# Kernel optimization log

Hardware: AMD Instinct MI355X
Metric: run time of the kernel (lower is better)

The kernel has to match this reference:

```python
import jax, jax.numpy as jnp
import numpy as np

B, N, F = 32, 1024, 7
HID, HID_GLO, MLP_H, OUT = 256, 8, 64, 8
THRESHOLD = 0.3


def setup_inputs() -> dict:
    key = jax.random.key(0)
    ks = jax.random.split(key, 16)
    def lin(k, fan_out, fan_in):
        # xavier-uniform-like init
        lim = (6.0 / (fan_in + fan_out)) ** 0.5
        return jax.random.uniform(k, (fan_out, fan_in), jnp.float32, -lim, lim)
    return {
        "x": jax.random.normal(ks[0], (B, N, F), jnp.float32),
        "W1": lin(ks[1], HID, 2),   "b1": jnp.zeros((HID,), jnp.float32),
        "W2": lin(ks[2], HID, HID), "b2": jnp.zeros((HID,), jnp.float32),
        "Wfc": lin(ks[3], HID, HID), "bfc": jnp.zeros((HID,), jnp.float32),
        "Wg": lin(ks[4], HID_GLO, 2), "bg": jnp.zeros((HID_GLO,), jnp.float32),
        "Wm0": lin(ks[5], MLP_H, N * F), "bm0": jnp.zeros((MLP_H,), jnp.float32),
        "Wm1": lin(ks[6], MLP_H, MLP_H), "bm1": jnp.zeros((MLP_H,), jnp.float32),
        "Wp": lin(ks[7], OUT, MLP_H + HID + HID_GLO), "bp": jnp.zeros((OUT,), jnp.float32),
    }


def reference(x, W1, b1, W2, b2, Wfc, bfc, Wg, bg, Wm0, bm0, Wm1, bm1, Wp, bp):
    # --- GCN branch (torch code detaches node features & adjacency) ---
    pts = jax.lax.stop_gradient(x[:, :, 1:3])                     # [B,N,2]
    diff = pts[:, :, None, :] - pts[:, None, :, :]                # [B,N,N,2]
    dist = jnp.sqrt(jnp.sum(diff * diff, axis=-1))                # [B,N,N]
    adj = (dist < THRESHOLD).astype(x.dtype)                      # [B,N,N]
    dinv = 1.0 / jnp.sqrt(jnp.sum(adj, axis=-1))                  # [B,N] (>=1, self-loop)
    nadj = dinv[:, :, None] * adj * dinv[:, None, :]              # D^-1/2 A D^-1/2
    h = jax.nn.relu(jnp.einsum('bij,bjd->bid', nadj, pts) @ W1.T + b1)   # [B,N,256]
    g = jnp.einsum('bij,bjh->bih', nadj, h) @ W2.T + b2                  # [B,N,256]
    gcn_en = jnp.mean(g, axis=1) @ Wfc.T + bfc                    # [B,256]

    # --- global branch (torch code uses .item() -> constants) ---
    v = jax.lax.stop_gradient(x[:, :, 1:5])                       # [B,N,4]
    avg_speed = jnp.mean(jnp.linalg.norm(v[:, :, 2:4], axis=-1), axis=1)  # [B]
    density = 1.0 / jnp.max(dist, axis=(1, 2))                    # [B] (v3 == pts)
    glo_in = jnp.stack([avg_speed, density], axis=-1)             # [B,2]
    glo_en = jax.nn.relu(glo_in @ Wg.T + bg)                      # [B,8]

    # --- MLP branch on flattened x ---
    xf = x.reshape(x.shape[0], -1)                                # [B, N*F]
    xf = jax.nn.relu(xf @ Wm0.T + bm0)
    xf = jax.nn.relu(xf @ Wm1.T + bm1)                            # [B,64]

    out = jnp.concatenate([xf, gcn_en, glo_en], axis=1) @ Wp.T + bp  # [B,8]
    return out
```

## Files before the change

kernel.cpp:

```cpp
#include <hip/hip_runtime.h>

#define NN 1024
#define FF 7
#define HID 256
#define MLPH 64
#define OUTN 8
#define CATN (MLPH + HID + 8)

__device__ __forceinline__ float wave_sum(float v) {
#pragma unroll
    for (int m = 32; m >= 1; m >>= 1) v += __shfl_xor(v, m, 64);
    return v;
}
__device__ __forceinline__ float wave_max(float v) {
#pragma unroll
    for (int m = 32; m >= 1; m >>= 1) v = fmaxf(v, __shfl_xor(v, m, 64));
    return v;
}

__global__ __launch_bounds__(512, 2) void g1(const float* __restrict__ x,
                                             const float* __restrict__ Wm0,
                                             const float* __restrict__ W2,
                                             const float* __restrict__ b2,
                                             const float* __restrict__ Wfc,
                                             const float* __restrict__ bfc,
                                             const float* __restrict__ Wp,
                                             float* __restrict__ spd,
                                             float* __restrict__ mlp_p,
                                             float* __restrict__ E,
                                             float* __restrict__ cE,
                                             float* __restrict__ deg,
                                             float* __restrict__ bmaxp,
                                             float* __restrict__ out) {
    __shared__ __align__(16) float lxs[NN * FF];
    __shared__ __align__(16) float l0[NN];
    __shared__ __align__(16) float l1[NN];
    __shared__ __align__(16) float s2[NN];
    __shared__ float wred[8];
    __shared__ float eg0[HID];
    __shared__ float eg1[HID];
    int blk = blockIdx.x, tid = threadIdx.x, lane = tid & 63, w = tid >> 6;
    int b = blk >> 3, jg = blk & 7;

    const float4* wr = (const float4*)(Wm0 + (jg * 8 + w) * (NN * FF));
    float4 wreg[28];
#pragma unroll
    for (int t = 0; t < 28; ++t) wreg[t] = wr[t * 64 + lane];
    const float4* xr4 = (const float4*)(x + b * (NN * FF));
    float4 xreg0 = xr4[tid];
    float4 xreg1 = xr4[512 + tid];
    float4 xreg2 = xr4[1024 + tid];
    float4 xreg3;
    if (tid < 256) xreg3 = xr4[1536 + tid];
    float4* lx4 = (float4*)lxs;
    lx4[tid] = xreg0;
    lx4[512 + tid] = xreg1;
    lx4[1024 + tid] = xreg2;
    if (tid < 256) lx4[1536 + tid] = xreg3;
    __syncthreads();
    l0[tid] = lxs[tid * 7 + 1];       l1[tid] = lxs[tid * 7 + 2];
    l0[tid + 512] = lxs[(tid + 512) * 7 + 1];
    l1[tid + 512] = lxs[(tid + 512) * 7 + 2];
    __syncthreads();
    int jA = jg * 128 + lane, jB = jA + 64;
    float pj0a = l0[jA], pj1a = l1[jA];
    float pj0b = l0[jB], pj1b = l1[jB];
    {
        const float4* v0p = (const float4*)&l0[w * 128];
        const float4* v1p = (const float4*)&l1[w * 128];
        unsigned dA = 0u, dB = 0u;
        float mx = 0.f;
#pragma unroll 4
        for (int g = 0; g < 32; ++g) {
            float4 v0 = v0p[g], v1 = v1p[g];
            float dx, dy, d2a, d2b;
            dx = pj0a - v0.x; dy = pj1a - v1.x; d2a = fmaf(dy, dy, dx * dx);
            dx = pj0b - v0.x; dy = pj1b - v1.x; d2b = fmaf(dy, dy, dx * dx);
            dA += (d2a <= 0.09f); dB += (d2b <= 0.09f);
            mx = fmaxf(mx, fmaxf(d2a, d2b));
            dx = pj0a - v0.y; dy = pj1a - v1.y; d2a = fmaf(dy, dy, dx * dx);
            dx = pj0b - v0.y; dy = pj1b - v1.y; d2b = fmaf(dy, dy, dx * dx);
            dA += (d2a <= 0.09f); dB += (d2b <= 0.09f);
            mx = fmaxf(mx, fmaxf(d2a, d2b));
            dx = pj0a - v0.z; dy = pj1a - v1.z; d2a = fmaf(dy, dy, dx * dx);
            dx = pj0b - v0.z; dy = pj1b - v1.z; d2b = fmaf(dy, dy, dx * dx);
            dA += (d2a <= 0.09f); dB += (d2b <= 0.09f);
            mx = fmaxf(mx, fmaxf(d2a, d2b));
            dx = pj0a - v0.w; dy = pj1a - v1.w; d2a = fmaf(dy, dy, dx * dx);
            dx = pj0b - v0.w; dy = pj1b - v1.w; d2b = fmaf(dy, dy, dx * dx);
            dA += (d2a <= 0.09f); dB += (d2b <= 0.09f);
            mx = fmaxf(mx, fmaxf(d2a, d2b));
        }
        s2[w * 128 + lane] = (float)dA;
        s2[w * 128 + 64 + lane] = (float)dB;
        mx = wave_max(mx);
        if (lane == 0) wred[w] = mx;
    }
    __syncthreads();
    if (tid < 128) {
        float s = 0.f;
#pragma unroll
        for (int kk = 0; kk < 8; ++kk) s += s2[kk * 128 + tid];
        deg[b * NN + jg * 128 + tid] = s;
    }
    if (tid == 0) {
        float m = wred[0];
#pragma unroll
        for (int i = 1; i < 8; ++i) m = fmaxf(m, wred[i]);
        bmaxp[b * 8 + jg] = m;
    }
    {
        float4 a4 = {0.f, 0.f, 0.f, 0.f};
#pragma unroll
        for (int t = 0; t < 28; ++t) {
            float4 xv = lx4[t * 64 + lane];
            a4.x = fmaf(wreg[t].x, xv.x, a4.x);
            a4.y = fmaf(wreg[t].y, xv.y, a4.y);
            a4.z = fmaf(wreg[t].z, xv.z, a4.z);
            a4.w = fmaf(wreg[t].w, xv.w, a4.w);
        }
        float s = (a4.x + a4.y) + (a4.z + a4.w);
        s = wave_sum(s);
        if (lane == 0) mlp_p[b * MLPH + jg * 8 + w] = s;
    }
    __syncthreads();
    if (jg == 0) {
        float vx = lxs[tid * 7 + 3], vy = lxs[tid * 7 + 4];
        float sp = sqrtf(fmaf(vx, vx, vy * vy));
        vx = lxs[(tid + 512) * 7 + 3]; vy = lxs[(tid + 512) * 7 + 4];
        sp += sqrtf(fmaf(vx, vx, vy * vy));
        sp = wave_sum(sp);
        if (lane == 0) wred[w] = sp;
        if (tid < OUTN) out[b * OUTN + tid] = 0.f;
    }
    __syncthreads();
    if (jg == 0 && tid == 0) {
        float s = 0.f;
#pragma unroll
        for (int i = 0; i < 8; ++i) s += wred[i];
        spd[b] = s;
    }
    if (b >= 8 && b < 16 && jg == 7) {
        int o = b - 8;
        int half = tid >> 8, col = tid & 255;
        float* hp = s2;
        if (tid < HID) eg0[tid] = Wp[o * CATN + MLPH + tid];
        __syncthreads();
        {
            float a = 0.f;
            const float* wcol = Wfc + (half * 128) * HID + col;
#pragma unroll 8
            for (int m = 0; m < 128; ++m) a = fmaf(eg0[half * 128 + m], wcol[m * HID], a);
            hp[tid] = a;
        }
        __syncthreads();
        if (tid < HID) eg1[tid] = hp[tid] + hp[tid + 256];
        __syncthreads();
        {
            float e = 0.f;
            const float* wcol = W2 + (half * 128) * HID + col;
#pragma unroll 8
            for (int k = 0; k < 128; ++k) e = fmaf(eg1[half * 128 + k], wcol[k * HID], e);
            hp[tid] = e;
        }
        __syncthreads();
        if (tid < HID) {
            E[o * HID + tid] = hp[tid] + hp[tid + 256];
            float c = fmaf(eg1[tid], b2[tid], eg0[tid] * bfc[tid]);
            c = wave_sum(c);
            if (lane == 0) wred[w] = c;
        }
        __syncthreads();
        if (tid == 0) cE[o] = wred[0] + wred[1] + wred[2] + wred[3];
    }
}

__global__ __launch_bounds__(512, 4) void g2(const float* __restrict__ x,
                                             const float* __restrict__ deg,
                                             const float* __restrict__ W1,
                                             const float* __restrict__ b1,
                                             const float* __restrict__ Wg,
                                             const float* __restrict__ bg,
                                             const float* __restrict__ Wm1,
                                             const float* __restrict__ bm1,
                                             const float* __restrict__ Wp,
                                             const float* __restrict__ bp,
                                             const float* __restrict__ bm0,
                                             const float* __restrict__ mlp_p,
                                             const float* __restrict__ bmaxp,
                                             const float* __restrict__ spd,
                                             const float* __restrict__ E,
                                             const float* __restrict__ cE,
                                             float* __restrict__ out) {
    __shared__ __align__(16) float l0[NN];
    __shared__ __align__(16) float l1[NN];
    __shared__ __align__(16) float di[NN];
    __shared__ __align__(16) float r0[8 * 128];
    __shared__ __align__(16) float r1[8 * 128];
    __shared__ __align__(16) float r2[8 * 128];
    __shared__ __align__(16) float q0s[128];
    __shared__ __align__(16) float q1s[128];
    __shared__ __align__(16) float qws[128];
    __shared__ __align__(16) float hp[512];
    __shared__ float sx1[MLPH], sxf2[MLPH], sglo[8];
    int blk = blockIdx.x, tid = threadIdx.x, lane = tid & 63, w = tid >> 6;
    int b = blk >> 3, jg = blk & 7;
    const float* xb = x + b * (NN * FF);
    {
        int j0 = tid, j1 = tid + 512;
        l0[j0] = xb[j0 * FF + 1]; l1[j0] = xb[j0 * FF + 2];
        l0[j1] = xb[j1 * FF + 1]; l1[j1] = xb[j1 * FF + 2];
        di[j0] = 1.0f / sqrtf(deg[b * NN + j0]);
        di[j1] = 1.0f / sqrtf(deg[b * NN + j1]);
    }
    __syncthreads();
    int jA = jg * 128 + lane, jB = jA + 64;
    float pj0a = l0[jA], pj1a = l1[jA];
    float pj0b = l0[jB], pj1b = l1[jB];
    const float4* v0p = (const float4*)&l0[w * 128];
    const float4* v1p = (const float4*)&l1[w * 128];
    const float4* vdp = (const float4*)&di[w * 128];
    float a0a = 0.f, a1a = 0.f, asa = 0.f;
    float a0b = 0.f, a1b = 0.f, asb = 0.f;
#pragma unroll 4
    for (int g = 0; g < 32; ++g) {
        float4 v0 = v0p[g], v1 = v1p[g], vd = vdp[g];
        float dx, dy, d2, t;
        dx = pj0a - v0.x; dy = pj1a - v1.x; d2 = fmaf(dy, dy, dx * dx);
        t = (d2 <= 0.09f) ? vd.x : 0.0f;
        a0a = fmaf(t, v0.x, a0a); a1a = fmaf(t, v1.x, a1a); asa += t;
        dx = pj0b - v0.x; dy = pj1b - v1.x; d2 = fmaf(dy, dy, dx * dx);
        t = (d2 <= 0.09f) ? vd.x : 0.0f;
        a0b = fmaf(t, v0.x, a0b); a1b = fmaf(t, v1.x, a1b); asb += t;
        dx = pj0a - v0.y; dy = pj1a - v1.y; d2 = fmaf(dy, dy, dx * dx);
        t = (d2 <= 0.09f) ? vd.y : 0.0f;
        a0a = fmaf(t, v0.y, a0a); a1a = fmaf(t, v1.y, a1a); asa += t;
        dx = pj0b - v0.y; dy = pj1b - v1.y; d2 = fmaf(dy, dy, dx * dx);
        t = (d2 <= 0.09f) ? vd.y : 0.0f;
        a0b = fmaf(t, v0.y, a0b); a1b = fmaf(t, v1.y, a1b); asb += t;
        dx = pj0a - v0.z; dy = pj1a - v1.z; d2 = fmaf(dy, dy, dx * dx);
        t = (d2 <= 0.09f) ? vd.z : 0.0f;
        a0a = fmaf(t, v0.z, a0a); a1a = fmaf(t, v1.z, a1a); asa += t;
        dx = pj0b - v0.z; dy = pj1b - v1.z; d2 = fmaf(dy, dy, dx * dx);
        t = (d2 <= 0.09f) ? vd.z : 0.0f;
        a0b = fmaf(t, v0.z, a0b); a1b = fmaf(t, v1.z, a1b); asb += t;
        dx = pj0a - v0.w; dy = pj1a - v1.w; d2 = fmaf(dy, dy, dx * dx);
        t = (d2 <= 0.09f) ? vd.w : 0.0f;
        a0a = fmaf(t, v0.w, a0a); a1a = fmaf(t, v1.w, a1a); asa += t;
        dx = pj0b - v0.w; dy = pj1b - v1.w; d2 = fmaf(dy, dy, dx * dx);
        t = (d2 <= 0.09f) ? vd.w : 0.0f;
        a0b = fmaf(t, v0.w, a0b); a1b = fmaf(t, v1.w, a1b); asb += t;
    }
    r0[w * 128 + lane] = a0a; r0[w * 128 + 64 + lane] = a0b;
    r1[w * 128 + lane] = a1a; r1[w * 128 + 64 + lane] = a1b;
    r2[w * 128 + lane] = asa; r2[w * 128 + 64 + lane] = asb;
    __syncthreads();
    if (tid < 128) {
        float s0 = 0.f, s1 = 0.f, ss = 0.f;
#pragma unroll
        for (int kk = 0; kk < 8; ++kk) {
            s0 += r0[kk * 128 + tid];
            s1 += r1[kk * 128 + tid];
            ss += r2[kk * 128 + tid];
        }
        float dj = di[jg * 128 + tid];
        q0s[tid] = dj * s0;
        q1s[tid] = dj * s1;
        qws[tid] = dj * ss * (1.0f / NN);
    } else if (jg == 0 && tid < 192) {
        int t2 = tid - 128;
        sx1[t2] = fmaxf(mlp_p[b * MLPH + t2] + bm0[t2], 0.f);
    }
    __syncthreads();
    {
        int h = tid & 255, jq = tid >> 8;
        float w10 = W1[2 * h], w11 = W1[2 * h + 1], bb = b1[h];
        const float4* q0v = (const float4*)&q0s[jq * 64];
        const float4* q1v = (const float4*)&q1s[jq * 64];
        const float4* qwv = (const float4*)&qws[jq * 64];
        float acc = 0.f;
#pragma unroll
        for (int g = 0; g < 16; ++g) {
            float4 qa = q0v[g], qb = q1v[g], qw4 = qwv[g];
            acc = fmaf(qw4.x, fmaxf(fmaf(qb.x, w11, fmaf(qa.x, w10, bb)), 0.f), acc);
            acc = fmaf(qw4.y, fmaxf(fmaf(qb.y, w11, fmaf(qa.y, w10, bb)), 0.f), acc);
            acc = fmaf(qw4.z, fmaxf(fmaf(qb.z, w11, fmaf(qa.z, w10, bb)), 0.f), acc);
            acc = fmaf(qw4.w, fmaxf(fmaf(qb.w, w11, fmaf(qa.w, w10, bb)), 0.f), acc);
        }
        hp[jq * 256 + h] = acc;
    }
    __syncthreads();
    if (tid < HID) {
        r0[tid] = hp[tid] + hp[256 + tid];
    } else if (jg == 0 && tid < HID + MLPH) {
        int t2 = tid - HID;
        float a = bm1[t2];
        const float* wv = Wm1 + t2 * MLPH;
#pragma unroll
        for (int k = 0; k < MLPH; ++k) a = fmaf(wv[k], sx1[k], a);
        sxf2[t2] = fmaxf(a, 0.f);
    } else if (jg == 0 && tid < HID + MLPH + 8) {
        int t2 = tid - HID - MLPH;
        float mxv = 0.f;
#pragma unroll
        for (int g = 0; g < 8; ++g) mxv = fmaxf(mxv, bmaxp[b * 8 + g]);
        float avg  = spd[b] * (1.0f / NN);
        float dens = 1.0f / sqrtf(mxv);
        sglo[t2] = fmaxf(fmaf(Wg[t2 * 2], avg, fmaf(Wg[t2 * 2 + 1], dens, bg[t2])), 0.f);
    }
    __syncthreads();
    {
        int o = w, ln = lane;
        const float* Eo = E + o * HID;
        float a = Eo[ln] * r0[ln];
        a = fmaf(Eo[ln + 64],  r0[ln + 64],  a);
        a = fmaf(Eo[ln + 128], r0[ln + 128], a);
        a = fmaf(Eo[ln + 192], r0[ln + 192], a);
        if (jg == 0) a = fmaf(Wp[o * CATN + ln], sxf2[ln], a);
        a = wave_sum(a);
        if (ln == 0) {
            if (jg == 0) {
                const float* wg = Wp + o * CATN + MLPH + HID;
#pragma unroll
                for (int g = 0; g < 8; ++g) a = fmaf(wg[g], sglo[g], a);
                a += cE[o] + bp[o];
            }
            atomicAdd(&out[b * OUTN + o], a);
        }
    }
}

extern "C" void kernel_launch(void* const* d_in, const int* in_sizes, int n_in,
                              void* d_out, int out_size, void* d_ws, size_t ws_size,
                              hipStream_t stream) {
    const float* x   = (const float*)d_in[0];
    const float* W1  = (const float*)d_in[1];
    const float* b1  = (const float*)d_in[2];
    const float* W2  = (const float*)d_in[3];
    const float* b2  = (const float*)d_in[4];
    const float* Wfc = (const float*)d_in[5];
    const float* bfc = (const float*)d_in[6];
    const float* Wg  = (const float*)d_in[7];
    const float* bg  = (const float*)d_in[8];
    const float* Wm0 = (const float*)d_in[9];
    const float* bm0 = (const float*)d_in[10];
    const float* Wm1 = (const float*)d_in[11];
    const float* bm1 = (const float*)d_in[12];
    const float* Wp  = (const float*)d_in[13];
    const float* bp  = (const float*)d_in[14];
    float* out = (float*)d_out;
    float* ws  = (float*)d_ws;

    float* deg   = ws;
    float* mlp_p = ws + 32768;
    float* bmaxp = ws + 34816;
    float* spd   = ws + 35072;
    float* E     = ws + 35104;
    float* cE    = ws + 37152;

    g1<<<256, 512, 0, stream>>>(x, Wm0, W2, b2, Wfc, bfc, Wp,
                                spd, mlp_p, E, cE, deg, bmaxp, out);
    g2<<<256, 512, 0, stream>>>(x, deg, W1, b1, Wg, bg, Wm1, bm1,
                                Wp, bp, bm0, mlp_p, bmaxp, spd, E, cE, out);
}
```

Measured before the change: 113.3 us.

## Fuse two kernels into one with per-batch spin-wait flags and inline W2/Wfc matvecs

Merges the two launches into a single kernel. The 8 blocks of each batch exchange degree, max-distance and MLP partials through global memory, gated by per-block release flags and a bounded spin-wait. The precomputed Wp·Wfc·W2 projection is dropped; each block now runs the W2 and Wfc matvecs on its own partial aggregate. This removes a launch gap and the serial E-precompute path, but relies on all 8 blocks of a batch being co-resident to avoid deadlock, and adds redundant per-block matvec work plus a hand-rolled release/acquire protocol whose ordering is delicate.

```diff
diff --git a/kernel.cpp b/kernel.cpp
--- a/kernel.cpp
+++ b/kernel.cpp
@@ -7,6 +7,9 @@
 #define OUTN 8
 #define CATN (MLPH + HID + 8)
 
+#define FMAGIC 0x9E3779B97F4A7C15ULL
+#define SCOPE_AGENT __HIP_MEMORY_SCOPE_AGENT
+
 __device__ __forceinline__ float wave_sum(float v) {
 #pragma unroll
     for (int m = 32; m >= 1; m >>= 1) v += __shfl_xor(v, m, 64);
@@ -17,30 +20,58 @@
     for (int m = 32; m >= 1; m >>= 1) v = fmaxf(v, __shfl_xor(v, m, 64));
     return v;
 }
-
-__global__ __launch_bounds__(512, 2) void g1(const float* __restrict__ x,
+__device__ __forceinline__ void st_ag(float* p, float v) {
+    __hip_atomic_store(p, v, __ATOMIC_RELAXED, SCOPE_AGENT);
+}
+__device__ __forceinline__ float ld_ag(const float* p) {
+    return __hip_atomic_load(p, __ATOMIC_RELAXED, SCOPE_AGENT);
+}
+
+union SU {
+    float lxs[NN * FF];
+    struct {
+        float r0[NN], r1[NN], r2[NN];
+        float q0s[128], q1s[128], qws[128];
+        float hp[512];
+        float yh[512];
+        float yv[HID];
+        float zv[HID];
+        float sx1[MLPH], sxf2[MLPH], sglo[8];
+    } p2;
+};
+
+__global__ __launch_bounds__(512, 2) void gf(const float* __restrict__ x,
                                              const float* __restrict__ Wm0,
                                              const float* __restrict__ W2,
                                              const float* __restrict__ b2,
                                              const float* __restrict__ Wfc,
                                              const float* __restrict__ bfc,
+                                             const float* __restrict__ W1,
+                                             const float* __restrict__ b1,
+                                             const float* __restrict__ Wg,
+                                             const float* __restrict__ bg,
+                                             const float* __restrict__ Wm1,
+                                             const float* __restrict__ bm1,
                                              const float* __restrict__ Wp,
-                                             float* __restrict__ spd,
+                                             const float* __restrict__ bp,
+                                             const float* __restrict__ bm0,
                                              float* __restrict__ mlp_p,
-                                             float* __restrict__ E,
-                                             float* __restrict__ cE,
                                              float* __restrict__ deg,
                                              float* __restrict__ bmaxp,
+                                             unsigned long long* __restrict__ flags,
                                              float* __restrict__ out) {
-    __shared__ __align__(16) float lxs[NN * FF];
+    __shared__ __align__(16) SU u;
     __shared__ __align__(16) float l0[NN];
     __shared__ __align__(16) float l1[NN];
+    __shared__ __align__(16) float di[NN];
     __shared__ __align__(16) float s2[NN];
     __shared__ float wred[8];
-    __shared__ float eg0[HID];
-    __shared__ float eg1[HID];
+    __shared__ float sspd;
+
     int blk = blockIdx.x, tid = threadIdx.x, lane = tid & 63, w = tid >> 6;
     int b = blk >> 3, jg = blk & 7;
+    unsigned long long* myflag = &flags[b * 8 + jg];
+    if (tid == 0) __hip_atomic_store(myflag, 0ULL, __ATOMIC_RELAXED, SCOPE_AGENT);
 
     const float4* wr = (const float4*)(Wm0 + (jg * 8 + w) * (NN * FF));
     float4 wreg[28];
@@ -52,15 +83,15 @@
     float4 xreg2 = xr4[1024 + tid];
     float4 xreg3;
     if (tid < 256) xreg3 = xr4[1536 + tid];
-    float4* lx4 = (float4*)lxs;
+    float4* lx4 = (float4*)u.lxs;
     lx4[tid] = xreg0;
     lx4[512 + tid] = xreg1;
     lx4[1024 + tid] = xreg2;
     if (tid < 256) lx4[1536 + tid] = xreg3;
     __syncthreads();
-    l0[tid] = lxs[tid * 7 + 1];       l1[tid] = lxs[tid * 7 + 2];
-    l0[tid + 512] = lxs[(tid + 512) * 7 + 1];
-    l1[tid + 512] = lxs[(tid + 512) * 7 + 2];
+    l0[tid] = u.lxs[tid * 7 + 1];       l1[tid] = u.lxs[tid * 7 + 2];
+    l0[tid + 512] = u.lxs[(tid + 512) * 7 + 1];
+    l1[tid + 512] = u.lxs[(tid + 512) * 7 + 2];
     __syncthreads();
     int jA = jg * 128 + lane, jB = jA + 64;
     float pj0a = l0[jA], pj1a = l1[jA];
@@ -101,13 +132,13 @@
         float s = 0.f;
 #pragma unroll
         for (int kk = 0; kk < 8; ++kk) s += s2[kk * 128 + tid];
-        deg[b * NN + jg * 128 + tid] = s;
+        st_ag(&deg[b * NN + jg * 128 + tid], s);
     }
     if (tid == 0) {
         float m = wred[0];
 #pragma unroll
         for (int i = 1; i < 8; ++i) m = fmaxf(m, wred[i]);
-        bmaxp[b * 8 + jg] = m;
+        st_ag(&bmaxp[b * 8 + jg], m);
     }
     {
         float4 a4 = {0.f, 0.f, 0.f, 0.f};
@@ -121,139 +152,84 @@
         }
         float s = (a4.x + a4.y) + (a4.z + a4.w);
         s = wave_sum(s);
-        if (lane == 0) mlp_p[b * MLPH + jg * 8 + w] = s;
+        if (lane == 0) st_ag(&mlp_p[b * MLPH + jg * 8 + w], s);
     }
     __syncthreads();
     if (jg == 0) {
-        float vx = lxs[tid * 7 + 3], vy = lxs[tid * 7 + 4];
+        float vx = u.lxs[tid * 7 + 3], vy = u.lxs[tid * 7 + 4];
         float sp = sqrtf(fmaf(vx, vx, vy * vy));
-        vx = lxs[(tid + 512) * 7 + 3]; vy = lxs[(tid + 512) * 7 + 4];
+        vx = u.lxs[(tid + 512) * 7 + 3]; vy = u.lxs[(tid + 512) * 7 + 4];
         sp += sqrtf(fmaf(vx, vx, vy * vy));
         sp = wave_sum(sp);
         if (lane == 0) wred[w] = sp;
-        if (tid < OUTN) out[b * OUTN + tid] = 0.f;
+        if (tid < OUTN) st_ag(&out[b * OUTN + tid], 0.f);
     }
     __syncthreads();
     if (jg == 0 && tid == 0) {
         float s = 0.f;
 #pragma unroll
         for (int i = 0; i < 8; ++i) s += wred[i];
-        spd[b] = s;
-    }
-    if (b >= 8 && b < 16 && jg == 7) {
-        int o = b - 8;
-        int half = tid >> 8, col = tid & 255;
-        float* hp = s2;
-        if (tid < HID) eg0[tid] = Wp[o * CATN + MLPH + tid];
-        __syncthreads();
-        {
-            float a = 0.f;
-            const float* wcol = Wfc + (half * 128) * HID + col;
-#pragma unroll 8
-            for (int m = 0; m < 128; ++m) a = fmaf(eg0[half * 128 + m], wcol[m * HID], a);
-            hp[tid] = a;
-        }
-        __syncthreads();
-        if (tid < HID) eg1[tid] = hp[tid] + hp[tid + 256];
-        __syncthreads();
-        {
-            float e = 0.f;
-            const float* wcol = W2 + (half * 128) * HID + col;
-#pragma unroll 8
-            for (int k = 0; k < 128; ++k) e = fmaf(eg1[half * 128 + k], wcol[k * HID], e);
-            hp[tid] = e;
-        }
-        __syncthreads();
-        if (tid < HID) {
-            E[o * HID + tid] = hp[tid] + hp[tid + 256];
-            float c = fmaf(eg1[tid], b2[tid], eg0[tid] * bfc[tid]);
-            c = wave_sum(c);
-            if (lane == 0) wred[w] = c;
-        }
-        __syncthreads();
-        if (tid == 0) cE[o] = wred[0] + wred[1] + wred[2] + wred[3];
-    }
-}
-
-__global__ __launch_bounds__(512, 4) void g2(const float* __restrict__ x,
-                                             const float* __restrict__ deg,
-                                             const float* __restrict__ W1,
-                                             const float* __restrict__ b1,
-                                             const float* __restrict__ Wg,
-                                             const float* __restrict__ bg,
-                                             const float* __restrict__ Wm1,
-                                             const float* __restrict__ bm1,
-                                             const float* __restrict__ Wp,
-                                             const float* __restrict__ bp,
-                                             const float* __restrict__ bm0,
-                                             const float* __restrict__ mlp_p,
-                                             const float* __restrict__ bmaxp,
-                                             const float* __restrict__ spd,
-                                             const float* __restrict__ E,
-                                             const float* __restrict__ cE,
-                                             float* __restrict__ out) {
-    __shared__ __align__(16) float l0[NN];
-    __shared__ __align__(16) float l1[NN];
-    __shared__ __align__(16) float di[NN];
-    __shared__ __align__(16) float r0[8 * 128];
-    __shared__ __align__(16) float r1[8 * 128];
-    __shared__ __align__(16) float r2[8 * 128];
-    __shared__ __align__(16) float q0s[128];
-    __shared__ __align__(16) float q1s[128];
-    __shared__ __align__(16) float qws[128];
-    __shared__ __align__(16) float hp[512];
-    __shared__ float sx1[MLPH], sxf2[MLPH], sglo[8];
-    int blk = blockIdx.x, tid = threadIdx.x, lane = tid & 63, w = tid >> 6;
-    int b = blk >> 3, jg = blk & 7;
-    const float* xb = x + b * (NN * FF);
-    {
-        int j0 = tid, j1 = tid + 512;
-        l0[j0] = xb[j0 * FF + 1]; l1[j0] = xb[j0 * FF + 2];
-        l0[j1] = xb[j1 * FF + 1]; l1[j1] = xb[j1 * FF + 2];
-        di[j0] = 1.0f / sqrtf(deg[b * NN + j0]);
-        di[j1] = 1.0f / sqrtf(deg[b * NN + j1]);
-    }
-    __syncthreads();
-    int jA = jg * 128 + lane, jB = jA + 64;
-    float pj0a = l0[jA], pj1a = l1[jA];
-    float pj0b = l0[jB], pj1b = l1[jB];
-    const float4* v0p = (const float4*)&l0[w * 128];
-    const float4* v1p = (const float4*)&l1[w * 128];
-    const float4* vdp = (const float4*)&di[w * 128];
-    float a0a = 0.f, a1a = 0.f, asa = 0.f;
-    float a0b = 0.f, a1b = 0.f, asb = 0.f;
+        sspd = s;
+    }
+    __syncthreads();
+    if (tid == 0)
+        __hip_atomic_store(myflag, FMAGIC, __ATOMIC_RELEASE, SCOPE_AGENT);
+
+    if (tid < 8) {
+        int it = 0;
+        while (__hip_atomic_load(&flags[b * 8 + tid], __ATOMIC_RELAXED,
+                                 SCOPE_AGENT) != FMAGIC && it < (1 << 20)) {
+            __builtin_amdgcn_s_sleep(2);
+            ++it;
+        }
+    }
+    __syncthreads();
+
+    di[tid]       = 1.0f / sqrtf(ld_ag(&deg[b * NN + tid]));
+    di[tid + 512] = 1.0f / sqrtf(ld_ag(&deg[b * NN + tid + 512]));
+    __syncthreads();
+    float* r0 = u.p2.r0;
+    float* r1 = u.p2.r1;
+    float* r2 = u.p2.r2;
+    {
+        const float4* v0p = (const float4*)&l0[w * 128];
+        const float4* v1p = (const float4*)&l1[w * 128];
+        const float4* vdp = (const float4*)&di[w * 128];
+        float a0a = 0.f, a1a = 0.f, asa = 0.f;
+        float a0b = 0.f, a1b = 0.f, asb = 0.f;
 #pragma unroll 4
-    for (int g = 0; g < 32; ++g) {
-        float4 v0 = v0p[g], v1 = v1p[g], vd = vdp[g];
-        float dx, dy, d2, t;
-        dx = pj0a - v0.x; dy = pj1a - v1.x; d2 = fmaf(dy, dy, dx * dx);
-        t = (d2 <= 0.09f) ? vd.x : 0.0f;
-        a0a = fmaf(t, v0.x, a0a); a1a = fmaf(t, v1.x, a1a); asa += t;
-        dx = pj0b - v0.x; dy = pj1b - v1.x; d2 = fmaf(dy, dy, dx * dx);
-        t = (d2 <= 0.09f) ? vd.x : 0.0f;
-        a0b = fmaf(t, v0.x, a0b); a1b = fmaf(t, v1.x, a1b); asb += t;
-        dx = pj0a - v0.y; dy = pj1a - v1.y; d2 = fmaf(dy, dy, dx * dx);
-        t = (d2 <= 0.09f) ? vd.y : 0.0f;
-        a0a = fmaf(t, v0.y, a0a); a1a = fmaf(t, v1.y, a1a); asa += t;
-        dx = pj0b - v0.y; dy = pj1b - v1.y; d2 = fmaf(dy, dy, dx * dx);
-        t = (d2 <= 0.09f) ? vd.y : 0.0f;
-        a0b = fmaf(t, v0.y, a0b); a1b = fmaf(t, v1.y, a1b); asb += t;
-        dx = pj0a - v0.z; dy = pj1a - v1.z; d2 = fmaf(dy, dy, dx * dx);
-        t = (d2 <= 0.09f) ? vd.z : 0.0f;
-        a0a = fmaf(t, v0.z, a0a); a1a = fmaf(t, v1.z, a1a); asa += t;
-        dx = pj0b - v0.z; dy = pj1b - v1.z; d2 = fmaf(dy, dy, dx * dx);
-        t = (d2 <= 0.09f) ? vd.z : 0.0f;
-        a0b = fmaf(t, v0.z, a0b); a1b = fmaf(t, v1.z, a1b); asb += t;
-        dx = pj0a - v0.w; dy = pj1a - v1.w; d2 = fmaf(dy, dy, dx * dx);
-        t = (d2 <= 0.09f) ? vd.w : 0.0f;
-        a0a = fmaf(t, v0.w, a0a); a1a = fmaf(t, v1.w, a1a); asa += t;
-        dx = pj0b - v0.w; dy = pj1b - v1.w; d2 = fmaf(dy, dy, dx * dx);
-        t = (d2 <= 0.09f) ? vd.w : 0.0f;
-        a0b = fmaf(t, v0.w, a0b); a1b = fmaf(t, v1.w, a1b); asb += t;
-    }
-    r0[w * 128 + lane] = a0a; r0[w * 128 + 64 + lane] = a0b;
-    r1[w * 128 + lane] = a1a; r1[w * 128 + 64 + lane] = a1b;
-    r2[w * 128 + lane] = asa; r2[w * 128 + 64 + lane] = asb;
+        for (int g = 0; g < 32; ++g) {
+            float4 v0 = v0p[g], v1 = v1p[g], vd = vdp[g];
+            float dx, dy, d2, t;
+            dx = pj0a - v0.x; dy = pj1a - v1.x; d2 = fmaf(dy, dy, dx * dx);
+            t = (d2 <= 0.09f) ? vd.x : 0.0f;
+            a0a = fmaf(t, v0.x, a0a); a1a = fmaf(t, v1.x, a1a); asa += t;
+            dx = pj0b - v0.x; dy = pj1b - v1.x; d2 = fmaf(dy, dy, dx * dx);
+            t = (d2 <= 0.09f) ? vd.x : 0.0f;
+            a0b = fmaf(t, v0.x, a0b); a1b = fmaf(t, v1.x, a1b); asb += t;
+            dx = pj0a - v0.y; dy = pj1a - v1.y; d2 = fmaf(dy, dy, dx * dx);
+            t = (d2 <= 0.09f) ? vd.y : 0.0f;
+            a0a = fmaf(t, v0.y, a0a); a1a = fmaf(t, v1.y, a1a); asa += t;
+            dx = pj0b - v0.y; dy = pj1b - v1.y; d2 = fmaf(dy, dy, dx * dx);
+            t = (d2 <= 0.09f) ? vd.y : 0.0f;
+            a0b = fmaf(t, v0.y, a0b); a1b = fmaf(t, v1.y, a1b); asb += t;
+            dx = pj0a - v0.z; dy = pj1a - v1.z; d2 = fmaf(dy, dy, dx * dx);
+            t = (d2 <= 0.09f) ? vd.z : 0.0f;
+            a0a = fmaf(t, v0.z, a0a); a1a = fmaf(t, v1.z, a1a); asa += t;
+            dx = pj0b - v0.z; dy = pj1b - v1.z; d2 = fmaf(dy, dy, dx * dx);
+            t = (d2 <= 0.09f) ? vd.z : 0.0f;
+            a0b = fmaf(t, v0.z, a0b); a1b = fmaf(t, v1.z, a1b); asb += t;
+            dx = pj0a - v0.w; dy = pj1a - v1.w; d2 = fmaf(dy, dy, dx * dx);
+            t = (d2 <= 0.09f) ? vd.w : 0.0f;
+            a0a = fmaf(t, v0.w, a0a); a1a = fmaf(t, v1.w, a1a); asa += t;
+            dx = pj0b - v0.w; dy = pj1b - v1.w; d2 = fmaf(dy, dy, dx * dx);
+            t = (d2 <= 0.09f) ? vd.w : 0.0f;
+            a0b = fmaf(t, v0.w, a0b); a1b = fmaf(t, v1.w, a1b); asb += t;
+        }
+        r0[w * 128 + lane] = a0a; r0[w * 128 + 64 + lane] = a0b;
+        r1[w * 128 + lane] = a1a; r1[w * 128 + 64 + lane] = a1b;
+        r2[w * 128 + lane] = asa; r2[w * 128 + 64 + lane] = asb;
+    }
     __syncthreads();
     if (tid < 128) {
         float s0 = 0.f, s1 = 0.f, ss = 0.f;
@@ -264,20 +240,20 @@
             ss += r2[kk * 128 + tid];
         }
         float dj = di[jg * 128 + tid];
-        q0s[tid] = dj * s0;
-        q1s[tid] = dj * s1;
-        qws[tid] = dj * ss * (1.0f / NN);
+        u.p2.q0s[tid] = dj * s0;
+        u.p2.q1s[tid] = dj * s1;
+        u.p2.qws[tid] = dj * ss * (1.0f / NN);
     } else if (jg == 0 && tid < 192) {
         int t2 = tid - 128;
-        sx1[t2] = fmaxf(mlp_p[b * MLPH + t2] + bm0[t2], 0.f);
+        u.p2.sx1[t2] = fmaxf(ld_ag(&mlp_p[b * MLPH + t2]) + bm0[t2], 0.f);
     }
     __syncthreads();
     {
         int h = tid & 255, jq = tid >> 8;
         float w10 = W1[2 * h], w11 = W1[2 * h + 1], bb = b1[h];
-        const float4* q0v = (const float4*)&q0s[jq * 64];
-        const float4* q1v = (const float4*)&q1s[jq * 64];
-        const float4* qwv = (const float4*)&qws[jq * 64];
+        const float4* q0v = (const float4*)&u.p2.q0s[jq * 64];
+        const float4* q1v = (const float4*)&u.p2.q1s[jq * 64];
+        const float4* qwv = (const float4*)&u.p2.qws[jq * 64];
         float acc = 0.f;
 #pragma unroll
         for (int g = 0; g < 16; ++g) {
@@ -287,43 +263,77 @@
             acc = fmaf(qw4.z, fmaxf(fmaf(qb.z, w11, fmaf(qa.z, w10, bb)), 0.f), acc);
             acc = fmaf(qw4.w, fmaxf(fmaf(qb.w, w11, fmaf(qa.w, w10, bb)), 0.f), acc);
         }
-        hp[jq * 256 + h] = acc;
+        u.p2.hp[jq * 256 + h] = acc;
     }
     __syncthreads();
     if (tid < HID) {
-        r0[tid] = hp[tid] + hp[256 + tid];
+        r0[tid] = u.p2.hp[tid] + u.p2.hp[256 + tid];
     } else if (jg == 0 && tid < HID + MLPH) {
         int t2 = tid - HID;
         float a = bm1[t2];
         const float* wv = Wm1 + t2 * MLPH;
 #pragma unroll
-        for (int k = 0; k < MLPH; ++k) a = fmaf(wv[k], sx1[k], a);
-        sxf2[t2] = fmaxf(a, 0.f);
+        for (int k = 0; k < MLPH; ++k) a = fmaf(wv[k], u.p2.sx1[k], a);
+        u.p2.sxf2[t2] = fmaxf(a, 0.f);
     } else if (jg == 0 && tid < HID + MLPH + 8) {
         int t2 = tid - HID - MLPH;
         float mxv = 0.f;
 #pragma unroll
-        for (int g = 0; g < 8; ++g) mxv = fmaxf(mxv, bmaxp[b * 8 + g]);
-        float avg  = spd[b] * (1.0f / NN);
+        for (int g = 0; g < 8; ++g) mxv = fmaxf(mxv, ld_ag(&bmaxp[b * 8 + g]));
+        float avg  = sspd * (1.0f / NN);
         float dens = 1.0f / sqrtf(mxv);
-        sglo[t2] = fmaxf(fmaf(Wg[t2 * 2], avg, fmaf(Wg[t2 * 2 + 1], dens, bg[t2])), 0.f);
-    }
+        u.p2.sglo[t2] = fmaxf(fmaf(Wg[t2 * 2], avg, fmaf(Wg[t2 * 2 + 1], dens, bg[t2])), 0.f);
+    }
+    __syncthreads();
+    {
+        int r = tid >> 1, half = tid & 1;
+        const float4* w4 = (const float4*)(W2 + r * HID + half * 128);
+        const float4* v4 = (const float4*)&r0[half * 128];
+        float acc = 0.f;
+#pragma unroll
+        for (int t = 0; t < 32; ++t) {
+            float4 a = w4[t], vv = v4[t];
+            acc = fmaf(a.x, vv.x, acc); acc = fmaf(a.y, vv.y, acc);
+            acc = fmaf(a.z, vv.z, acc); acc = fmaf(a.w, vv.w, acc);
+        }
+        u.p2.yh[tid] = acc;
+    }
+    __syncthreads();
+    if (tid < HID)
+        u.p2.yv[tid] = u.p2.yh[2 * tid] + u.p2.yh[2 * tid + 1] + (jg == 0 ? b2[tid] : 0.f);
+    __syncthreads();
+    {
+        int r = tid >> 1, half = tid & 1;
+        const float4* w4 = (const float4*)(Wfc + r * HID + half * 128);
+        const float4* v4 = (const float4*)&u.p2.yv[half * 128];
+        float acc = 0.f;
+#pragma unroll
+        for (int t = 0; t < 32; ++t) {
+            float4 a = w4[t], vv = v4[t];
+            acc = fmaf(a.x, vv.x, acc); acc = fmaf(a.y, vv.y, acc);
+            acc = fmaf(a.z, vv.z, acc); acc = fmaf(a.w, vv.w, acc);
+        }
+        u.p2.yh[tid] = acc;
+    }
+    __syncthreads();
+    if (tid < HID)
+        u.p2.zv[tid] = u.p2.yh[2 * tid] + u.p2.yh[2 * tid + 1] + (jg == 0 ? bfc[tid] : 0.f);
     __syncthreads();
     {
         int o = w, ln = lane;
-        const float* Eo = E + o * HID;
-        float a = Eo[ln] * r0[ln];
-        a = fmaf(Eo[ln + 64],  r0[ln + 64],  a);
-        a = fmaf(Eo[ln + 128], r0[ln + 128], a);
-        a = fmaf(Eo[ln + 192], r0[ln + 192], a);
-        if (jg == 0) a = fmaf(Wp[o * CATN + ln], sxf2[ln], a);
+        const float* wpo = Wp + o * CATN;
+        float a = wpo[MLPH + ln] * u.p2.zv[ln];
+        a = fmaf(wpo[MLPH + ln + 64],  u.p2.zv[ln + 64],  a);
+        a = fmaf(wpo[MLPH + ln + 128], u.p2.zv[ln + 128], a);
+        a = fmaf(wpo[MLPH + ln + 192], u.p2.zv[ln + 192], a);
+        if (jg == 0) a = fmaf(wpo[ln], u.p2.sxf2[ln], a);
         a = wave_sum(a);
         if (ln == 0) {
             if (jg == 0) {
-                const float* wg = Wp + o * CATN + MLPH + HID;
-#pragma unroll
-                for (int g = 0; g < 8; ++g) a = fmaf(wg[g], sglo[g], a);
-                a += cE[o] + bp[o];
+                const float* wg = wpo + MLPH + HID;
+#pragma unroll
+                for (int g = 0; g < 8; ++g) a = fmaf(wg[g], u.p2.sglo[g], a);
+                a += bp[o];
             }
             atomicAdd(&out[b * OUTN + o], a);
         }
@@ -354,12 +364,9 @@
     float* deg   = ws;
     float* mlp_p = ws + 32768;
     float* bmaxp = ws + 34816;
-    float* spd   = ws + 35072;
-    float* E     = ws + 35104;
-    float* cE    = ws + 37152;
-
-    g1<<<256, 512, 0, stream>>>(x, Wm0, W2, b2, Wfc, bfc, Wp,
-                                spd, mlp_p, E, cE, deg, bmaxp, out);
-    g2<<<256, 512, 0, stream>>>(x, deg, W1, b1, Wg, bg, Wm1, bm1,
-                                Wp, bp, bm0, mlp_p, bmaxp, spd, E, cE, out);
-}
+    unsigned long long* flags = (unsigned long long*)(ws + 35072);
+
+    gf<<<256, 512, 0, stream>>>(x, Wm0, W2, b2, Wfc, bfc, W1, b1, Wg, bg,
+                                Wm1, bm1, Wp, bp, bm0,
+                                mlp_p, deg, bmaxp, flags, out);
+}
```

Result: slower. 120.0 us (+5.9%).

## Double grid to 16 blocks per batch and stage packed point coordinates

Applied to the files above, without the earlier changes.

Both kernels now use 16 blocks per batch with 64 target nodes each instead of 8 blocks with 128, which halves per-thread work and register use (Wm0 register tile shrinks from 28 to 14 float4). g1 writes de-interleaved x/y coordinates to workspace so g2 can load them with coalesced float4 reads instead of strided gathers from x. The intent is more parallelism and occupancy on a small problem, at the cost of redundantly recomputing all pairwise distances in more blocks and running more partial reductions and atomics.

```diff
diff --git a/kernel.cpp b/kernel.cpp
--- a/kernel.cpp
+++ b/kernel.cpp
@@ -18,7 +18,7 @@
     return v;
 }
 
-__global__ __launch_bounds__(512, 2) void g1(const float* __restrict__ x,
+__global__ __launch_bounds__(512, 4) void g1(const float* __restrict__ x,
                                              const float* __restrict__ Wm0,
                                              const float* __restrict__ W2,
                                              const float* __restrict__ b2,
@@ -31,89 +31,79 @@
                                              float* __restrict__ cE,
                                              float* __restrict__ deg,
                                              float* __restrict__ bmaxp,
+                                             float* __restrict__ pts0,
+                                             float* __restrict__ pts1,
                                              float* __restrict__ out) {
     __shared__ __align__(16) float lxs[NN * FF];
     __shared__ __align__(16) float l0[NN];
     __shared__ __align__(16) float l1[NN];
-    __shared__ __align__(16) float s2[NN];
+    __shared__ __align__(16) float s2[512];
     __shared__ float wred[8];
-    __shared__ float eg0[HID];
-    __shared__ float eg1[HID];
+    __shared__ float mred[8];
+    __shared__ float eg0[HID], eg1[HID];
     int blk = blockIdx.x, tid = threadIdx.x, lane = tid & 63, w = tid >> 6;
-    int b = blk >> 3, jg = blk & 7;
-
-    const float4* wr = (const float4*)(Wm0 + (jg * 8 + w) * (NN * FF));
-    float4 wreg[28];
-#pragma unroll
-    for (int t = 0; t < 28; ++t) wreg[t] = wr[t * 64 + lane];
+    int b = blk >> 4, jq = blk & 15;
+
+    int hrow = jq * 4 + (w >> 1), hsel = w & 1;
+    const float4* wr = (const float4*)(Wm0 + hrow * (NN * FF)) + hsel * 896;
+    float4 wreg[14];
+#pragma unroll
+    for (int t = 0; t < 14; ++t) wreg[t] = wr[t * 64 + lane];
     const float4* xr4 = (const float4*)(x + b * (NN * FF));
-    float4 xreg0 = xr4[tid];
-    float4 xreg1 = xr4[512 + tid];
-    float4 xreg2 = xr4[1024 + tid];
-    float4 xreg3;
-    if (tid < 256) xreg3 = xr4[1536 + tid];
+    float4 x0 = xr4[tid], x1 = xr4[512 + tid], x2 = xr4[1024 + tid], x3;
+    if (tid < 256) x3 = xr4[1536 + tid];
     float4* lx4 = (float4*)lxs;
-    lx4[tid] = xreg0;
-    lx4[512 + tid] = xreg1;
-    lx4[1024 + tid] = xreg2;
-    if (tid < 256) lx4[1536 + tid] = xreg3;
-    __syncthreads();
-    l0[tid] = lxs[tid * 7 + 1];       l1[tid] = lxs[tid * 7 + 2];
+    lx4[tid] = x0;
+    lx4[512 + tid] = x1;
+    lx4[1024 + tid] = x2;
+    if (tid < 256) lx4[1536 + tid] = x3;
+    __syncthreads();
+    l0[tid] = lxs[tid * 7 + 1];        l1[tid] = lxs[tid * 7 + 2];
     l0[tid + 512] = lxs[(tid + 512) * 7 + 1];
     l1[tid + 512] = lxs[(tid + 512) * 7 + 2];
     __syncthreads();
-    int jA = jg * 128 + lane, jB = jA + 64;
-    float pj0a = l0[jA], pj1a = l1[jA];
-    float pj0b = l0[jB], pj1b = l1[jB];
+    int j = jq * 64 + lane;
+    float pj0 = l0[j], pj1 = l1[j];
     {
         const float4* v0p = (const float4*)&l0[w * 128];
         const float4* v1p = (const float4*)&l1[w * 128];
-        unsigned dA = 0u, dB = 0u;
+        unsigned dA = 0u;
         float mx = 0.f;
 #pragma unroll 4
         for (int g = 0; g < 32; ++g) {
             float4 v0 = v0p[g], v1 = v1p[g];
-            float dx, dy, d2a, d2b;
-            dx = pj0a - v0.x; dy = pj1a - v1.x; d2a = fmaf(dy, dy, dx * dx);
-            dx = pj0b - v0.x; dy = pj1b - v1.x; d2b = fmaf(dy, dy, dx * dx);
-            dA += (d2a <= 0.09f); dB += (d2b <= 0.09f);
-            mx = fmaxf(mx, fmaxf(d2a, d2b));
-            dx = pj0a - v0.y; dy = pj1a - v1.y; d2a = fmaf(dy, dy, dx * dx);
-            dx = pj0b - v0.y; dy = pj1b - v1.y; d2b = fmaf(dy, dy, dx * dx);
-            dA += (d2a <= 0.09f); dB += (d2b <= 0.09f);
-            mx = fmaxf(mx, fmaxf(d2a, d2b));
-            dx = pj0a - v0.z; dy = pj1a - v1.z; d2a = fmaf(dy, dy, dx * dx);
-            dx = pj0b - v0.z; dy = pj1b - v1.z; d2b = fmaf(dy, dy, dx * dx);
-            dA += (d2a <= 0.09f); dB += (d2b <= 0.09f);
-            mx = fmaxf(mx, fmaxf(d2a, d2b));
-            dx = pj0a - v0.w; dy = pj1a - v1.w; d2a = fmaf(dy, dy, dx * dx);
-            dx = pj0b - v0.w; dy = pj1b - v1.w; d2b = fmaf(dy, dy, dx * dx);
-            dA += (d2a <= 0.09f); dB += (d2b <= 0.09f);
-            mx = fmaxf(mx, fmaxf(d2a, d2b));
-        }
-        s2[w * 128 + lane] = (float)dA;
-        s2[w * 128 + 64 + lane] = (float)dB;
+            float dx, dy, d2;
+            dx = pj0 - v0.x; dy = pj1 - v1.x; d2 = fmaf(dy, dy, dx * dx);
+            dA += (d2 <= 0.09f); mx = fmaxf(mx, d2);
+            dx = pj0 - v0.y; dy = pj1 - v1.y; d2 = fmaf(dy, dy, dx * dx);
+            dA += (d2 <= 0.09f); mx = fmaxf(mx, d2);
+            dx = pj0 - v0.z; dy = pj1 - v1.z; d2 = fmaf(dy, dy, dx * dx);
+            dA += (d2 <= 0.09f); mx = fmaxf(mx, d2);
+            dx = pj0 - v0.w; dy = pj1 - v1.w; d2 = fmaf(dy, dy, dx * dx);
+            dA += (d2 <= 0.09f); mx = fmaxf(mx, d2);
+        }
+        s2[w * 64 + lane] = (float)dA;
         mx = wave_max(mx);
         if (lane == 0) wred[w] = mx;
     }
     __syncthreads();
-    if (tid < 128) {
+    if (tid < 64) {
         float s = 0.f;
 #pragma unroll
-        for (int kk = 0; kk < 8; ++kk) s += s2[kk * 128 + tid];
-        deg[b * NN + jg * 128 + tid] = s;
+        for (int kk = 0; kk < 8; ++kk) s += s2[kk * 64 + tid];
+        deg[b * NN + jq * 64 + tid] = s;
     }
     if (tid == 0) {
         float m = wred[0];
 #pragma unroll
         for (int i = 1; i < 8; ++i) m = fmaxf(m, wred[i]);
-        bmaxp[b * 8 + jg] = m;
+        bmaxp[b * 16 + jq] = m;
     }
     {
         float4 a4 = {0.f, 0.f, 0.f, 0.f};
 #pragma unroll
-        for (int t = 0; t < 28; ++t) {
-            float4 xv = lx4[t * 64 + lane];
+        for (int t = 0; t < 14; ++t) {
+            float4 xv = lx4[hsel * 896 + t * 64 + lane];
             a4.x = fmaf(wreg[t].x, xv.x, a4.x);
             a4.y = fmaf(wreg[t].y, xv.y, a4.y);
             a4.z = fmaf(wreg[t].z, xv.z, a4.z);
@@ -121,10 +111,12 @@
         }
         float s = (a4.x + a4.y) + (a4.z + a4.w);
         s = wave_sum(s);
-        if (lane == 0) mlp_p[b * MLPH + jg * 8 + w] = s;
-    }
-    __syncthreads();
-    if (jg == 0) {
+        if (lane == 0) mred[w] = s;
+    }
+    __syncthreads();
+    if ((w & 1) == 0 && lane == 0)
+        mlp_p[b * MLPH + hrow] = mred[w] + mred[w + 1];
+    if (jq == 0) {
         float vx = lxs[tid * 7 + 3], vy = lxs[tid * 7 + 4];
         float sp = sqrtf(fmaf(vx, vx, vy * vy));
         vx = lxs[(tid + 512) * 7 + 3]; vy = lxs[(tid + 512) * 7 + 4];
@@ -132,15 +124,19 @@
         sp = wave_sum(sp);
         if (lane == 0) wred[w] = sp;
         if (tid < OUTN) out[b * OUTN + tid] = 0.f;
-    }
-    __syncthreads();
-    if (jg == 0 && tid == 0) {
+        if (tid < 256) {
+            ((float4*)(pts0 + b * NN))[tid] = ((float4*)l0)[tid];
+            ((float4*)(pts1 + b * NN))[tid] = ((float4*)l1)[tid];
+        }
+    }
+    __syncthreads();
+    if (jq == 0 && tid == 0) {
         float s = 0.f;
 #pragma unroll
         for (int i = 0; i < 8; ++i) s += wred[i];
         spd[b] = s;
     }
-    if (b >= 8 && b < 16 && jg == 7) {
+    if (b >= 8 && b < 16 && jq == 15) {
         int o = b - 8;
         int half = tid >> 8, col = tid & 255;
         float* hp = s2;
@@ -175,7 +171,8 @@
     }
 }
 
-__global__ __launch_bounds__(512, 4) void g2(const float* __restrict__ x,
+__global__ __launch_bounds__(512, 4) void g2(const float* __restrict__ pts0,
+                                             const float* __restrict__ pts1,
                                              const float* __restrict__ deg,
                                              const float* __restrict__ W1,
                                              const float* __restrict__ b1,
@@ -195,115 +192,104 @@
     __shared__ __align__(16) float l0[NN];
     __shared__ __align__(16) float l1[NN];
     __shared__ __align__(16) float di[NN];
-    __shared__ __align__(16) float r0[8 * 128];
-    __shared__ __align__(16) float r1[8 * 128];
-    __shared__ __align__(16) float r2[8 * 128];
-    __shared__ __align__(16) float q0s[128];
-    __shared__ __align__(16) float q1s[128];
-    __shared__ __align__(16) float qws[128];
+    __shared__ __align__(16) float r0[512];
+    __shared__ __align__(16) float r1[512];
+    __shared__ __align__(16) float r2[512];
+    __shared__ __align__(16) float q0s[64];
+    __shared__ __align__(16) float q1s[64];
+    __shared__ __align__(16) float qws[64];
     __shared__ __align__(16) float hp[512];
     __shared__ float sx1[MLPH], sxf2[MLPH], sglo[8];
     int blk = blockIdx.x, tid = threadIdx.x, lane = tid & 63, w = tid >> 6;
-    int b = blk >> 3, jg = blk & 7;
-    const float* xb = x + b * (NN * FF);
-    {
-        int j0 = tid, j1 = tid + 512;
-        l0[j0] = xb[j0 * FF + 1]; l1[j0] = xb[j0 * FF + 2];
-        l0[j1] = xb[j1 * FF + 1]; l1[j1] = xb[j1 * FF + 2];
-        di[j0] = 1.0f / sqrtf(deg[b * NN + j0]);
-        di[j1] = 1.0f / sqrtf(deg[b * NN + j1]);
-    }
-    __syncthreads();
-    int jA = jg * 128 + lane, jB = jA + 64;
-    float pj0a = l0[jA], pj1a = l1[jA];
-    float pj0b = l0[jB], pj1b = l1[jB];
-    const float4* v0p = (const float4*)&l0[w * 128];
-    const float4* v1p = (const float4*)&l1[w * 128];
-    const float4* vdp = (const float4*)&di[w * 128];
-    float a0a = 0.f, a1a = 0.f, asa = 0.f;
-    float a0b = 0.f, a1b = 0.f, asb = 0.f;
+    int b = blk >> 4, jq = blk & 15;
+    if (tid < 256) {
+        ((float4*)l0)[tid] = ((const float4*)(pts0 + b * NN))[tid];
+        ((float4*)di)[tid] = ((const float4*)(deg + b * NN))[tid];
+    } else {
+        ((float4*)l1)[tid - 256] = ((const float4*)(pts1 + b * NN))[tid - 256];
+    }
+    __syncthreads();
+    di[tid] = 1.0f / sqrtf(di[tid]);
+    di[tid + 512] = 1.0f / sqrtf(di[tid + 512]);
+    __syncthreads();
+    int j = jq * 64 + lane;
+    float pj0 = l0[j], pj1 = l1[j];
+    {
+        const float4* v0p = (const float4*)&l0[w * 128];
+        const float4* v1p = (const float4*)&l1[w * 128];
+        const float4* vdp = (const float4*)&di[w * 128];
+        float a0 = 0.f, a1 = 0.f, as = 0.f;
 #pragma unroll 4
-    for (int g = 0; g < 32; ++g) {
-        float4 v0 = v0p[g], v1 = v1p[g], vd = vdp[g];
-        float dx, dy, d2, t;
-        dx = pj0a - v0.x; dy = pj1a - v1.x; d2 = fmaf(dy, dy, dx * dx);
-        t = (d2 <= 0.09f) ? vd.x : 0.0f;
-        a0a = fmaf(t, v0.x, a0a); a1a = fmaf(t, v1.x, a1a); asa += t;
-        dx = pj0b - v0.x; dy = pj1b - v1.x; d2 = fmaf(dy, dy, dx * dx);
-        t = (d2 <= 0.09f) ? vd.x : 0.0f;
-        a0b = fmaf(t, v0.x, a0b); a1b = fmaf(t, v1.x, a1b); asb += t;
-        dx = pj0a - v0.y; dy = pj1a - v1.y; d2 = fmaf(dy, dy, dx * dx);
-        t = (d2 <= 0.09f) ? vd.y : 0.0f;
-        a0a = fmaf(t, v0.y, a0a); a1a = fmaf(t, v1.y, a1a); asa += t;
-        dx = pj0b - v0.y; dy = pj1b - v1.y; d2 = fmaf(dy, dy, dx * dx);
-        t = (d2 <= 0.09f) ? vd.y : 0.0f;
-        a0b = fmaf(t, v0.y, a0b); a1b = fmaf(t, v1.y, a1b); asb += t;
-        dx = pj0a - v0.z; dy = pj1a - v1.z; d2 = fmaf(dy, dy, dx * dx);
-        t = (d2 <= 0.09f) ? vd.z : 0.0f;
-        a0a = fmaf(t, v0.z, a0a); a1a = fmaf(t, v1.z, a1a); asa += t;
-        dx = pj0b - v0.z; dy = pj1b - v1.z; d2 = fmaf(dy, dy, dx * dx);
-        t = (d2 <= 0.09f) ? vd.z : 0.0f;
-        a0b = fmaf(t, v0.z, a0b); a1b = fmaf(t, v1.z, a1b); asb += t;
-        dx = pj0a - v0.w; dy = pj1a - v1.w; d2 = fmaf(dy, dy, dx * dx);
-        t = (d2 <= 0.09f) ? vd.w : 0.0f;
-        a0a = fmaf(t, v0.w, a0a); a1a = fmaf(t, v1.w, a1a); asa += t;
-        dx = pj0b - v0.w; dy = pj1b - v1.w; d2 = fmaf(dy, dy, dx * dx);
-        t = (d2 <= 0.09f) ? vd.w : 0.0f;
-        a0b = fmaf(t, v0.w, a0b); a1b = fmaf(t, v1.w, a1b); asb += t;
-    }
-    r0[w * 128 + lane] = a0a; r0[w * 128 + 64 + lane] = a0b;
-    r1[w * 128 + lane] = a1a; r1[w * 128 + 64 + lane] = a1b;
-    r2[w * 128 + lane] = asa; r2[w * 128 + 64 + lane] = asb;
-    __syncthreads();
-    if (tid < 128) {
+        for (int g = 0; g < 32; ++g) {
+            float4 v0 = v0p[g], v1 = v1p[g], vd = vdp[g];
+            float dx, dy, d2, t;
+            dx = pj0 - v0.x; dy = pj1 - v1.x; d2 = fmaf(dy, dy, dx * dx);
+            t = (d2 <= 0.09f) ? vd.x : 0.0f;
+            a0 = fmaf(t, v0.x, a0); a1 = fmaf(t, v1.x, a1); as += t;
+            dx = pj0 - v0.y; dy = pj1 - v1.y; d2 = fmaf(dy, dy, dx * dx);
+            t = (d2 <= 0.09f) ? vd.y : 0.0f;
+            a0 = fmaf(t, v0.y, a0); a1 = fmaf(t, v1.y, a1); as += t;
+            dx = pj0 - v0.z; dy = pj1 - v1.z; d2 = fmaf(dy, dy, dx * dx);
+            t = (d2 <= 0.09f) ? vd.z : 0.0f;
+            a0 = fmaf(t, v0.z, a0); a1 = fmaf(t, v1.z, a1); as += t;
+            dx = pj0 - v0.w; dy = pj1 - v1.w; d2 = fmaf(dy, dy, dx * dx);
+            t = (d2 <= 0.09f) ? vd.w : 0.0f;
+            a0 = fmaf(t, v0.w, a0); a1 = fmaf(t, v1.w, a1); as += t;
+        }
+        r0[w * 64 + lane] = a0;
+        r1[w * 64 + lane] = a1;
+        r2[w * 64 + lane] = as;
+    }
+    __syncthreads();
+    if (tid < 64) {
         float s0 = 0.f, s1 = 0.f, ss = 0.f;
 #pragma unroll
         for (int kk = 0; kk < 8; ++kk) {
-            s0 += r0[kk * 128 + tid];
-            s1 += r1[kk * 128 + tid];
-            ss += r2[kk * 128 + tid];
-        }
-        float dj = di[jg * 128 + tid];
+            s0 += r0[kk * 64 + tid];
+            s1 += r1[kk * 64 + tid];
+            ss += r2[kk * 64 + tid];
+        }
+        float dj = di[jq * 64 + tid];
         q0s[tid] = dj * s0;
         q1s[tid] = dj * s1;
         qws[tid] = dj * ss * (1.0f / NN);
-    } else if (jg == 0 && tid < 192) {
-        int t2 = tid - 128;
+    } else if (jq == 0 && tid < 128) {
+        int t2 = tid - 64;
         sx1[t2] = fmaxf(mlp_p[b * MLPH + t2] + bm0[t2], 0.f);
     }
     __syncthreads();
     {
-        int h = tid & 255, jq = tid >> 8;
+        int h = tid & 255, jq2 = tid >> 8;
         float w10 = W1[2 * h], w11 = W1[2 * h + 1], bb = b1[h];
-        const float4* q0v = (const float4*)&q0s[jq * 64];
-        const float4* q1v = (const float4*)&q1s[jq * 64];
-        const float4* qwv = (const float4*)&qws[jq * 64];
+        const float4* q0v = (const float4*)&q0s[jq2 * 32];
+        const float4* q1v = (const float4*)&q1s[jq2 * 32];
+        const float4* qwv = (const float4*)&qws[jq2 * 32];
         float acc = 0.f;
 #pragma unroll
-        for (int g = 0; g < 16; ++g) {
+        for (int g = 0; g < 8; ++g) {
             float4 qa = q0v[g], qb = q1v[g], qw4 = qwv[g];
             acc = fmaf(qw4.x, fmaxf(fmaf(qb.x, w11, fmaf(qa.x, w10, bb)), 0.f), acc);
             acc = fmaf(qw4.y, fmaxf(fmaf(qb.y, w11, fmaf(qa.y, w10, bb)), 0.f), acc);
             acc = fmaf(qw4.z, fmaxf(fmaf(qb.z, w11, fmaf(qa.z, w10, bb)), 0.f), acc);
             acc = fmaf(qw4.w, fmaxf(fmaf(qb.w, w11, fmaf(qa.w, w10, bb)), 0.f), acc);
         }
-        hp[jq * 256 + h] = acc;
+        hp[jq2 * 256 + h] = acc;
     }
     __syncthreads();
     if (tid < HID) {
         r0[tid] = hp[tid] + hp[256 + tid];
-    } else if (jg == 0 && tid < HID + MLPH) {
+    } else if (jq == 0 && tid < HID + MLPH) {
         int t2 = tid - HID;
         float a = bm1[t2];
         const float* wv = Wm1 + t2 * MLPH;
 #pragma unroll
         for (int k = 0; k < MLPH; ++k) a = fmaf(wv[k], sx1[k], a);
         sxf2[t2] = fmaxf(a, 0.f);
-    } else if (jg == 0 && tid < HID + MLPH + 8) {
+    } else if (jq == 0 && tid < HID + MLPH + 8) {
         int t2 = tid - HID - MLPH;
         float mxv = 0.f;
 #pragma unroll
-        for (int g = 0; g < 8; ++g) mxv = fmaxf(mxv, bmaxp[b * 8 + g]);
+        for (int g = 0; g < 16; ++g) mxv = fmaxf(mxv, bmaxp[b * 16 + g]);
         float avg  = spd[b] * (1.0f / NN);
         float dens = 1.0f / sqrtf(mxv);
         sglo[t2] = fmaxf(fmaf(Wg[t2 * 2], avg, fmaf(Wg[t2 * 2 + 1], dens, bg[t2])), 0.f);
@@ -316,10 +302,10 @@
         a = fmaf(Eo[ln + 64],  r0[ln + 64],  a);
         a = fmaf(Eo[ln + 128], r0[ln + 128], a);
         a = fmaf(Eo[ln + 192], r0[ln + 192], a);
-        if (jg == 0) a = fmaf(Wp[o * CATN + ln], sxf2[ln], a);
+        if (jq == 0) a = fmaf(Wp[o * CATN + ln], sxf2[ln], a);
         a = wave_sum(a);
         if (ln == 0) {
-            if (jg == 0) {
+            if (jq == 0) {
                 const float* wg = Wp + o * CATN + MLPH + HID;
 #pragma unroll
                 for (int g = 0; g < 8; ++g) a = fmaf(wg[g], sglo[g], a);
@@ -354,12 +340,14 @@
     float* deg   = ws;
     float* mlp_p = ws + 32768;
     float* bmaxp = ws + 34816;
-    float* spd   = ws + 35072;
-    float* E     = ws + 35104;
-    float* cE    = ws + 37152;
-
-    g1<<<256, 512, 0, stream>>>(x, Wm0, W2, b2, Wfc, bfc, Wp,
-                                spd, mlp_p, E, cE, deg, bmaxp, out);
-    g2<<<256, 512, 0, stream>>>(x, deg, W1, b1, Wg, bg, Wm1, bm1,
+    float* spd   = ws + 35328;
+    float* E     = ws + 35360;
+    float* cE    = ws + 37408;
+    float* pts0  = ws + 37440;
+    float* pts1  = ws + 70208;
+
+    g1<<<512, 512, 0, stream>>>(x, Wm0, W2, b2, Wfc, bfc, Wp,
+                                spd, mlp_p, E, cE, deg, bmaxp, pts0, pts1, out);
+    g2<<<512, 512, 0, stream>>>(pts0, pts1, deg, W1, b1, Wg, bg, Wm1, bm1,
                                 Wp, bp, bm0, mlp_p, bmaxp, spd, E, cE, out);
 }
```

After: 113.9 us. About the same (+0.5%).
